# Optimization experiments

Measured on AMD Instinct MI355X. Metric: run time of the kernel, lower is better.

The kernel has to match this reference:

```python
import jax, jax.numpy as jnp
import numpy as np

B, N, C, H = 8, 1024, 768, 12
D = C // H  # head dim
SCALE = D ** -0.5


def setup_inputs() -> dict:
    key = jax.random.key(0)
    ks = jax.random.split(key, 5)
    return {
        "x": jax.random.normal(ks[0], (B, N, C), dtype=jnp.float32),
        "W_qkv": jax.random.normal(ks[1], (C, 3 * C), dtype=jnp.float32) * (C ** -0.5),
        "b_qkv": jax.random.normal(ks[2], (3 * C,), dtype=jnp.float32) * 0.02,
        "W_proj": jax.random.normal(ks[3], (C, C), dtype=jnp.float32) * (C ** -0.5),
        "b_proj": jax.random.normal(ks[4], (C,), dtype=jnp.float32) * 0.02,
    }


def reference(x, W_qkv, b_qkv, W_proj, b_proj):
    b, n, c = x.shape
    qkv = x @ W_qkv + b_qkv                      # [B,N,3C]
    # rearrange 'b n (k h c) -> k b h n c'
    qkv = qkv.reshape(b, n, 3, H, D).transpose(2, 0, 3, 1, 4)
    q, k, v = qkv[0] * SCALE, qkv[1], qkv[2]     # each [B,H,N,D]
    p = jax.nn.softmax(jnp.einsum('bhnd,bhmd->bhnm', q, k), axis=-1)
    o = jnp.einsum('bhnm,bhmd->bhnd', p, v)      # [B,H,N,D]
    o = o.transpose(0, 2, 1, 3).reshape(b, n, c)  # 'b h n c -> b n (h c)'
    return o @ W_proj + b_proj
```

## Files before the change

kernel.cpp:

```cpp
#include <hip/hip_runtime.h>


typedef short  bf16x8_t __attribute__((ext_vector_type(8)));
typedef float  f32x4_t  __attribute__((ext_vector_type(4)));

static __device__ __forceinline__ unsigned short f2bf(float f) {
    union { float f; unsigned u; } v; v.f = f;
    unsigned r = v.u + 0x7fffu + ((v.u >> 16) & 1u);
    return (unsigned short)(r >> 16);
}

typedef __attribute__((address_space(1))) const unsigned gas_u32;
typedef __attribute__((address_space(3))) unsigned las_u32;
static __device__ __forceinline__ void gload16(const void* g, void* l) {
    __builtin_amdgcn_global_load_lds((gas_u32*)g, (las_u32*)l, 16, 0, 0);
}

#define WAIT0 asm volatile("s_waitcnt vmcnt(0)" ::: "memory")
#define BAR   __builtin_amdgcn_s_barrier()

#define STAGE_TILE(DST, SRC, K0, NP, NT)                                   \
    _Pragma("unroll")                                                      \
    for (int p_ = 0; p_ < NP; ++p_) {                                      \
        const int base_ = p_*NT + wb;                                      \
        const int i_ = base_ + lane;                                       \
        const int row_ = i_ >> 3;                                          \
        const int cb_ = ((i_ & 7) ^ (row_ & 7)) * 8;                       \
        gload16((SRC) + (size_t)row_*768 + (K0) + cb_, &(DST)[base_*8]);   \
    }

#define COMPUTE_P(AS, BS)                                                  \
    {                                                                      \
        bf16x8_t a_[2][2], b_[2][4];                                       \
        _Pragma("unroll")                                                  \
        for (int ks_ = 0; ks_ < 2; ++ks_) {                                \
            _Pragma("unroll")                                              \
            for (int m_ = 0; m_ < 2; ++m_) {                               \
                const int ra_ = wm*32 + m_*16 + l15;                       \
                a_[ks_][m_] = *(const bf16x8_t*)&(AS)[ra_*64 + ((ks_*4 + lhi) ^ (ra_ & 7))*8]; \
            }                                                              \
            _Pragma("unroll")                                              \
            for (int n_ = 0; n_ < 4; ++n_) {                               \
                const int rb_ = wn*64 + n_*16 + l15;                       \
                b_[ks_][n_] = *(const bf16x8_t*)&(BS)[rb_*64 + ((ks_*4 + lhi) ^ (rb_ & 7))*8]; \
            }                                                              \
        }                                                                  \
        _Pragma("unroll")                                                  \
        for (int m_ = 0; m_ < 2; ++m_)                                     \
            _Pragma("unroll")                                              \
            for (int n_ = 0; n_ < 4; ++n_) {                               \
                acc[m_][n_] = __builtin_amdgcn_mfma_f32_16x16x32_bf16(a_[0][m_], b_[0][n_], acc[m_][n_], 0, 0, 0); \
                acc[m_][n_] = __builtin_amdgcn_mfma_f32_16x16x32_bf16(a_[1][m_], b_[1][n_], acc[m_][n_], 0, 0, 0); \
            }                                                              \
    }

__global__ __launch_bounds__(256) void convert_x(
    const float* __restrict__ src, unsigned short* __restrict__ dst)
{
    const int i = blockIdx.x * 256 + threadIdx.x;
    const float4 v = ((const float4*)src)[i];
    ushort4 o; o.x = f2bf(v.x); o.y = f2bf(v.y); o.z = f2bf(v.z); o.w = f2bf(v.w);
    ((ushort4*)dst)[i] = o;
}

__global__ __launch_bounds__(256) void transpose_cvt(
    const float* __restrict__ src, unsigned short* __restrict__ dst, int R, int C)
{
    __shared__ unsigned short tile[32][33];
    const int tx = threadIdx.x & 31, ty = threadIdx.x >> 5;
    const int bx = blockIdx.x, by = blockIdx.y;
    #pragma unroll
    for (int j = 0; j < 32; j += 8)
        tile[ty + j][tx] = f2bf(src[(size_t)(by*32 + ty + j) * C + bx*32 + tx]);
    __syncthreads();
    #pragma unroll
    for (int j = 0; j < 32; j += 8)
        dst[(size_t)(bx*32 + ty + j) * R + by*32 + tx] = tile[tx][ty + j];
}

__global__ __launch_bounds__(256, 4) void gemm_qkv_bf16(
    const unsigned short* __restrict__ A, const unsigned short* __restrict__ Bt,
    const float* __restrict__ bias,
    unsigned short* __restrict__ q, unsigned short* __restrict__ kO,
    unsigned short* __restrict__ vT)
{
    __shared__ unsigned short As[64*64];
    __shared__ unsigned short Bs[128*64];
    const int tid = threadIdx.x;
    const int id = blockIdx.x;
    const int xcd = id & 7, r = id >> 3;
    const int nb = r >> 4;
    const int mb = (r & 15) * 8 + xcd;
    const int n0 = nb * 128, m0 = mb * 64;

    const int lane = tid & 63, w = tid >> 6;
    const int l15 = lane & 15, lhi = lane >> 4;
    const int wm = w >> 1, wn = w & 1;
    const int wb = tid & 192;

    const unsigned short* Ab = A  + (size_t)m0 * 768;
    const unsigned short* Bb = Bt + (size_t)n0 * 768;

    f32x4_t acc[2][4] = {};

    #pragma unroll 1
    for (int t = 0; t < 12; ++t) {
        STAGE_TILE(As, Ab, t*64, 2, 256)
        STAGE_TILE(Bs, Bb, t*64, 4, 256)
        WAIT0; BAR;
        COMPUTE_P(As, Bs)
        BAR;
    }

    #pragma unroll
    for (int n = 0; n < 4; ++n) {
        const int gcol = n0 + wn*64 + n*16 + l15;
        const int kk = gcol / 768;
        const int rr = gcol - kk*768;
        const int h  = rr >> 6, d = rr & 63;
        const float bv = bias[gcol];
        const float sc = (kk == 0) ? 0.125f : 1.0f;
        #pragma unroll
        for (int m = 0; m < 2; ++m) {
            const int grow_base = m0 + wm*32 + m*16 + lhi*4;
            #pragma unroll
            for (int reg = 0; reg < 4; ++reg) {
                const int grow = grow_base + reg;
                const int bb = grow >> 10, seq = grow & 1023;
                const unsigned short ov = f2bf((acc[m][n][reg] + bv) * sc);
                const size_t bh = (size_t)bb*12 + h;
                if (kk == 0)      q [ (bh*1024 + seq)*64 + d ] = ov;
                else if (kk == 1) kO[ (bh*1024 + seq)*64 + d ] = ov;
                else              vT[ (bh*64 + d)*1024 + seq ] = ov;
            }
        }
    }
}

__global__ __launch_bounds__(256, 5) void attn2(
    const unsigned short* __restrict__ q, const unsigned short* __restrict__ k,
    const unsigned short* __restrict__ vT, unsigned short* __restrict__ obuf)
{
    __shared__ unsigned short Ks[64 * 72];
    __shared__ unsigned short Vs[64 * 72];
    __shared__ unsigned short P[4][16 * 72];
    const int tid = threadIdx.x;
    const int id = blockIdx.x;
    const int swz = (id & 7) * 192 + (id >> 3);
    const int qt = swz & 15, bh = swz >> 4;

    const int lane = tid & 63, w = tid >> 6;
    const int l15 = lane & 15, lhi = lane >> 4;
    const unsigned short* qp = q  + (size_t)bh * 65536;
    const unsigned short* kp = k  + (size_t)bh * 65536;
    const unsigned short* vp = vT + (size_t)bh * 65536;

    bf16x8_t qf[2];
    const int qrow = qt*64 + w*16 + l15;
    #pragma unroll
    for (int ks = 0; ks < 2; ++ks)
        qf[ks] = *(const bf16x8_t*)(qp + (size_t)qrow*64 + ks*32 + lhi*8);

    f32x4_t acco[4] = {};
    float lsum[4] = {0.f, 0.f, 0.f, 0.f};
    unsigned short* Pw = P[w];

    bf16x8_t kr[2], vr[2];
    #pragma unroll
    for (int p = 0; p < 2; ++p) {
        const int idx = p*256 + tid;
        const int r8 = idx >> 3, cb = (idx & 7) * 8;
        kr[p] = *(const bf16x8_t*)(kp + (size_t)r8*64 + cb);
        vr[p] = *(const bf16x8_t*)(vp + (size_t)r8*1024 + cb);
    }
    #pragma unroll
    for (int p = 0; p < 2; ++p) {
        const int idx = p*256 + tid;
        const int r8 = idx >> 3, cb = (idx & 7) * 8;
        *(bf16x8_t*)&Ks[r8*72 + cb] = kr[p];
        *(bf16x8_t*)&Vs[r8*72 + cb] = vr[p];
    }

    for (int kt = 0; kt < 16; ++kt) {
        __syncthreads();
        if (kt < 15) {
            #pragma unroll
            for (int p = 0; p < 2; ++p) {
                const int idx = p*256 + tid;
                const int r8 = idx >> 3, cb = (idx & 7) * 8;
                kr[p] = *(const bf16x8_t*)(kp + (size_t)((kt+1)*64 + r8)*64 + cb);
                vr[p] = *(const bf16x8_t*)(vp + (size_t)r8*1024 + (kt+1)*64 + cb);
            }
        }

        f32x4_t accs[4] = {};
        __builtin_amdgcn_s_setprio(1);
        #pragma unroll
        for (int c = 0; c < 4; ++c)
            #pragma unroll
            for (int ks = 0; ks < 2; ++ks) {
                bf16x8_t kf = *(const bf16x8_t*)&Ks[(c*16 + l15)*72 + ks*32 + lhi*8];
                accs[c] = __builtin_amdgcn_mfma_f32_16x16x32_bf16(qf[ks], kf, accs[c], 0, 0, 0);
            }
        __builtin_amdgcn_s_setprio(0);

        #pragma unroll
        for (int c = 0; c < 4; ++c)
            #pragma unroll
            for (int r = 0; r < 4; ++r) {
                const float pv = __expf(accs[c][r]);
                lsum[r] += pv;
                Pw[(lhi*4 + r)*72 + c*16 + l15] = f2bf(pv);
            }

        bf16x8_t pf[2];
        #pragma unroll
        for (int ks = 0; ks < 2; ++ks)
            pf[ks] = *(const bf16x8_t*)&Pw[l15*72 + ks*32 + lhi*8];
        __builtin_amdgcn_s_setprio(1);
        #pragma unroll
        for (int n = 0; n < 4; ++n)
            #pragma unroll
            for (int ks = 0; ks < 2; ++ks) {
                bf16x8_t vf = *(const bf16x8_t*)&Vs[(n*16 + l15)*72 + ks*32 + lhi*8];
                acco[n] = __builtin_amdgcn_mfma_f32_16x16x32_bf16(pf[ks], vf, acco[n], 0, 0, 0);
            }
        __builtin_amdgcn_s_setprio(0);

        __syncthreads();
        if (kt < 15) {
            #pragma unroll
            for (int p = 0; p < 2; ++p) {
                const int idx = p*256 + tid;
                const int r8 = idx >> 3, cb = (idx & 7) * 8;
                *(bf16x8_t*)&Ks[r8*72 + cb] = kr[p];
                *(bf16x8_t*)&Vs[r8*72 + cb] = vr[p];
            }
        }
    }

    #pragma unroll
    for (int r = 0; r < 4; ++r)
        #pragma unroll
        for (int off = 1; off <= 8; off <<= 1)
            lsum[r] += __shfl_xor(lsum[r], off, 64);

    const int b = bh / 12, h = bh % 12;
    #pragma unroll
    for (int n = 0; n < 4; ++n)
        #pragma unroll
        for (int r = 0; r < 4; ++r) {
            const int seq = qt*64 + w*16 + lhi*4 + r;
            obuf[((size_t)(b*1024 + seq))*768 + h*64 + n*16 + l15] = f2bf(acco[n][r] / lsum[r]);
        }
}

__global__ __launch_bounds__(256, 4) void gemm_proj_bf16(
    const unsigned short* __restrict__ A, const unsigned short* __restrict__ Bt,
    const float* __restrict__ bias, float* __restrict__ out)
{
    __shared__ unsigned short As[64*64];
    __shared__ unsigned short Bs[128*64];
    const int tid = threadIdx.x;
    const int id = blockIdx.x;
    const int swz = (id & 7) * 96 + (id >> 3);
    const int n0 = (swz % 6) * 128, m0 = (swz / 6) * 64;

    const int lane = tid & 63, w = tid >> 6;
    const int l15 = lane & 15, lhi = lane >> 4;
    const int wm = w >> 1, wn = w & 1;
    const int wb = tid & 192;

    const unsigned short* Ab = A  + (size_t)m0 * 768;
    const unsigned short* Bb = Bt + (size_t)n0 * 768;

    f32x4_t acc[2][4] = {};

    #pragma unroll 1
    for (int t = 0; t < 12; ++t) {
        STAGE_TILE(As, Ab, t*64, 2, 256)
        STAGE_TILE(Bs, Bb, t*64, 4, 256)
        WAIT0; BAR;
        COMPUTE_P(As, Bs)
        BAR;
    }

    #pragma unroll
    for (int n = 0; n < 4; ++n) {
        const int gcol = n0 + wn*64 + n*16 + l15;
        const float bv = bias[gcol];
        #pragma unroll
        for (int m = 0; m < 2; ++m) {
            const int grow_base = m0 + wm*32 + m*16 + lhi*4;
            #pragma unroll
            for (int reg = 0; reg < 4; ++reg)
                out[(size_t)(grow_base + reg)*768 + gcol] = acc[m][n][reg] + bv;
        }
    }
}

extern "C" void kernel_launch(void* const* d_in, const int* in_sizes, int n_in,
                              void* d_out, int out_size, void* d_ws, size_t ws_size,
                              hipStream_t stream) {
    const float* x     = (const float*)d_in[0];
    const float* Wqkv  = (const float*)d_in[1];
    const float* bqkv  = (const float*)d_in[2];
    const float* Wproj = (const float*)d_in[3];
    const float* bproj = (const float*)d_in[4];
    float* out = (float*)d_out;
    unsigned short* ws = (unsigned short*)d_ws;

    unsigned short* xb    = ws;
    unsigned short* obuf  = ws;
    unsigned short* wqt   = ws + 6291456u;
    unsigned short* wpt   = ws + 8060928u;
    unsigned short* qb    = ws + 8650752u;
    unsigned short* kb    = ws + 14942208u;
    unsigned short* vTb   = ws + 21233664u;

    convert_x     <<<6144, 256, 0, stream>>>(x, xb);
    transpose_cvt <<<dim3(72, 24), 256, 0, stream>>>(Wqkv, wqt, 768, 2304);
    transpose_cvt <<<dim3(24, 24), 256, 0, stream>>>(Wproj, wpt, 768, 768);
    gemm_qkv_bf16 <<<2304, 256, 0, stream>>>(xb, wqt, bqkv, qb, kb, vTb);
    attn2         <<<1536, 256, 0, stream>>>(qb, kb, vTb, obuf);
    gemm_proj_bf16<<<768,  256, 0, stream>>>(obuf, wpt, bproj, out);
}
```

Before: 130.1 us.

## Use 128-row query tiles with 8 waves in attention and raise GEMM occupancy

Attention blocks grow from 256 to 512 threads, so each block covers 128 query rows and shares each staged K/V tile across 8 waves instead of 4. This halves K/V global traffic and the number of blocks, and each thread now stages a single 16-byte chunk per tile. The launch-bounds occupancy hints for both GEMMs rise from 4 to 6 waves per SIMD, which may force register limits and spills. The larger blocks also mean fewer blocks per CU and coarser scheduling.

```diff
diff --git a/kernel.cpp b/kernel.cpp
--- a/kernel.cpp
+++ b/kernel.cpp
@@ -78,7 +78,7 @@
         dst[(size_t)(bx*32 + ty + j) * R + by*32 + tx] = tile[tx][ty + j];
 }
 
-__global__ __launch_bounds__(256, 4) void gemm_qkv_bf16(
+__global__ __launch_bounds__(256, 6) void gemm_qkv_bf16(
     const unsigned short* __restrict__ A, const unsigned short* __restrict__ Bt,
     const float* __restrict__ bias,
     unsigned short* __restrict__ q, unsigned short* __restrict__ kO,
@@ -137,17 +137,17 @@
     }
 }
 
-__global__ __launch_bounds__(256, 5) void attn2(
+__global__ __launch_bounds__(512, 6) void attn2(
     const unsigned short* __restrict__ q, const unsigned short* __restrict__ k,
     const unsigned short* __restrict__ vT, unsigned short* __restrict__ obuf)
 {
     __shared__ unsigned short Ks[64 * 72];
     __shared__ unsigned short Vs[64 * 72];
-    __shared__ unsigned short P[4][16 * 72];
+    __shared__ unsigned short P[8][16 * 72];
     const int tid = threadIdx.x;
     const int id = blockIdx.x;
-    const int swz = (id & 7) * 192 + (id >> 3);
-    const int qt = swz & 15, bh = swz >> 4;
+    const int swz = (id & 7) * 96 + (id >> 3);
+    const int qt = swz & 7, bh = swz >> 3;
 
     const int lane = tid & 63, w = tid >> 6;
     const int l15 = lane & 15, lhi = lane >> 4;
@@ -156,7 +156,7 @@
     const unsigned short* vp = vT + (size_t)bh * 65536;
 
     bf16x8_t qf[2];
-    const int qrow = qt*64 + w*16 + l15;
+    const int qrow = qt*128 + w*16 + l15;
     #pragma unroll
     for (int ks = 0; ks < 2; ++ks)
         qf[ks] = *(const bf16x8_t*)(qp + (size_t)qrow*64 + ks*32 + lhi*8);
@@ -165,32 +165,18 @@
     float lsum[4] = {0.f, 0.f, 0.f, 0.f};
     unsigned short* Pw = P[w];
 
-    bf16x8_t kr[2], vr[2];
-    #pragma unroll
-    for (int p = 0; p < 2; ++p) {
-        const int idx = p*256 + tid;
-        const int r8 = idx >> 3, cb = (idx & 7) * 8;
-        kr[p] = *(const bf16x8_t*)(kp + (size_t)r8*64 + cb);
-        vr[p] = *(const bf16x8_t*)(vp + (size_t)r8*1024 + cb);
-    }
-    #pragma unroll
-    for (int p = 0; p < 2; ++p) {
-        const int idx = p*256 + tid;
-        const int r8 = idx >> 3, cb = (idx & 7) * 8;
-        *(bf16x8_t*)&Ks[r8*72 + cb] = kr[p];
-        *(bf16x8_t*)&Vs[r8*72 + cb] = vr[p];
-    }
+    const int r8 = tid >> 3, cb = (tid & 7) * 8;
+    bf16x8_t kr, vr;
+    kr = *(const bf16x8_t*)(kp + (size_t)r8*64 + cb);
+    vr = *(const bf16x8_t*)(vp + (size_t)r8*1024 + cb);
+    *(bf16x8_t*)&Ks[r8*72 + cb] = kr;
+    *(bf16x8_t*)&Vs[r8*72 + cb] = vr;
 
     for (int kt = 0; kt < 16; ++kt) {
         __syncthreads();
         if (kt < 15) {
-            #pragma unroll
-            for (int p = 0; p < 2; ++p) {
-                const int idx = p*256 + tid;
-                const int r8 = idx >> 3, cb = (idx & 7) * 8;
-                kr[p] = *(const bf16x8_t*)(kp + (size_t)((kt+1)*64 + r8)*64 + cb);
-                vr[p] = *(const bf16x8_t*)(vp + (size_t)r8*1024 + (kt+1)*64 + cb);
-            }
+            kr = *(const bf16x8_t*)(kp + (size_t)((kt+1)*64 + r8)*64 + cb);
+            vr = *(const bf16x8_t*)(vp + (size_t)r8*1024 + (kt+1)*64 + cb);
         }
 
         f32x4_t accs[4] = {};
@@ -229,13 +215,8 @@
 
         __syncthreads();
         if (kt < 15) {
-            #pragma unroll
-            for (int p = 0; p < 2; ++p) {
-                const int idx = p*256 + tid;
-                const int r8 = idx >> 3, cb = (idx & 7) * 8;
-                *(bf16x8_t*)&Ks[r8*72 + cb] = kr[p];
-                *(bf16x8_t*)&Vs[r8*72 + cb] = vr[p];
-            }
+            *(bf16x8_t*)&Ks[r8*72 + cb] = kr;
+            *(bf16x8_t*)&Vs[r8*72 + cb] = vr;
         }
     }
 
@@ -250,12 +231,12 @@
     for (int n = 0; n < 4; ++n)
         #pragma unroll
         for (int r = 0; r < 4; ++r) {
-            const int seq = qt*64 + w*16 + lhi*4 + r;
+            const int seq = qt*128 + w*16 + lhi*4 + r;
             obuf[((size_t)(b*1024 + seq))*768 + h*64 + n*16 + l15] = f2bf(acco[n][r] / lsum[r]);
         }
 }
 
-__global__ __launch_bounds__(256, 4) void gemm_proj_bf16(
+__global__ __launch_bounds__(256, 6) void gemm_proj_bf16(
     const unsigned short* __restrict__ A, const unsigned short* __restrict__ Bt,
     const float* __restrict__ bias, float* __restrict__ out)
 {
@@ -322,6 +303,6 @@
     transpose_cvt <<<dim3(72, 24), 256, 0, stream>>>(Wqkv, wqt, 768, 2304);
     transpose_cvt <<<dim3(24, 24), 256, 0, stream>>>(Wproj, wpt, 768, 768);
     gemm_qkv_bf16 <<<2304, 256, 0, stream>>>(xb, wqt, bqkv, qb, kb, vTb);
-    attn2         <<<1536, 256, 0, stream>>>(qb, kb, vTb, obuf);
+    attn2         <<<768,  512, 0, stream>>>(qb, kb, vTb, obuf);
     gemm_proj_bf16<<<768,  256, 0, stream>>>(obuf, wpt, bproj, out);
 }
```

Measured after the change: 125.5 us. -3.5%, faster.
